# Kernel tuning notes

Hardware: AMD Instinct MI355X
Metric: run time of the kernel (lower is better)

The kernel has to match this reference:

```python
import jax, jax.numpy as jnp
import numpy as np

N = 10000        # nodes
E = 160000       # edges (before self loops)
F_IN = 4         # n_features
D = 128          # d_model (per-head out channels for GAT, GCN width)
H = 8            # n_heads
NEG_SLOPE = 0.2  # PyG GATConv default leaky relu slope


def setup_inputs() -> dict:
    key = jax.random.key(0)
    ks = jax.random.split(key, 10)
    x = jax.random.normal(ks[0], (N, F_IN), dtype=jnp.float32)
    edge_index = jax.random.randint(ks[1], (2, E), 0, N, dtype=jnp.int64)
    s = 0.05
    gat_w = jax.random.normal(ks[2], (F_IN, H * D), dtype=jnp.float32) * s
    att_src = jax.random.normal(ks[3], (H, D), dtype=jnp.float32) * s
    att_dst = jax.random.normal(ks[4], (H, D), dtype=jnp.float32) * s
    gat_b = jnp.zeros((H * D,), dtype=jnp.float32)
    gcn1_w = jax.random.normal(ks[5], (H * D, D), dtype=jnp.float32) * s
    gcn1_b = jnp.zeros((D,), dtype=jnp.float32)
    gcn2_w = jax.random.normal(ks[6], (D, D), dtype=jnp.float32) * s
    gcn2_b = jnp.zeros((D,), dtype=jnp.float32)
    return {"x": x, "edge_index": edge_index, "gat_w": gat_w,
            "att_src": att_src, "att_dst": att_dst, "gat_b": gat_b,
            "gcn1_w": gcn1_w, "gcn1_b": gcn1_b,
            "gcn2_w": gcn2_w, "gcn2_b": gcn2_b}


def _add_self_loops(edge_index, n):
    loops = jnp.arange(n, dtype=edge_index.dtype)
    src = jnp.concatenate([edge_index[0], loops])
    dst = jnp.concatenate([edge_index[1], loops])
    return src, dst


def _gat_conv(x, src, dst, w, att_src, att_dst, b):
    # PyG GATConv, concat=True: h [N,H,D]
    h = (x @ w).reshape(-1, H, D)
    a_s = jnp.einsum('nhd,hd->nh', h, att_src)   # per-node src score
    a_d = jnp.einsum('nhd,hd->nh', h, att_dst)   # per-node dst score
    e = jax.nn.leaky_relu(a_s[src] + a_d[dst], NEG_SLOPE)  # [Etot,H]
    # segment softmax over destination node, per head
    m = jax.ops.segment_max(e, dst, num_segments=N)
    ex = jnp.exp(e - m[dst])
    denom = jax.ops.segment_sum(ex, dst, num_segments=N)
    alpha = ex / denom[dst]                       # [Etot,H]
    msg = h[src] * alpha[:, :, None]              # [Etot,H,D]
    out = jax.ops.segment_sum(msg, dst, num_segments=N)  # [N,H,D]
    return out.reshape(-1, H * D) + b


def _gcn_conv(x, src, dst, w, b):
    # PyG GCNConv with symmetric normalization (self loops already added)
    h = x @ w
    deg = jax.ops.segment_sum(jnp.ones_like(dst, dtype=h.dtype), dst,
                              num_segments=N)
    dinv = jnp.where(deg > 0, jax.lax.rsqrt(deg), 0.0)
    norm = dinv[src] * dinv[dst]                  # [Etot]
    out = jax.ops.segment_sum(h[src] * norm[:, None], dst, num_segments=N)
    return out + b


def reference(x, edge_index, gat_w, att_src, att_dst, gat_b,
              gcn1_w, gcn1_b, gcn2_w, gcn2_b):
    src, dst = _add_self_loops(edge_index, N)
    h = _gat_conv(x, src, dst, gat_w, att_src, att_dst, gat_b)
    h = jax.nn.gelu(h, approximate=False)         # torch F.gelu is exact erf
    h = _gcn_conv(h, src, dst, gcn1_w, gcn1_b)
    h = jax.nn.gelu(h, approximate=False)
    h = _gcn_conv(h, src, dst, gcn2_w, gcn2_b)
    return h                                      # [N, D]
```

## Files before the change

### kernel.cpp

```cpp
#include <hip/hip_runtime.h>
#include <math.h>

#define HEADS 8
#define DHEAD 128
#define CMODEL 1024
#define BCAP 64

typedef __attribute__((ext_vector_type(8))) short bf16x8;
typedef __attribute__((ext_vector_type(4))) float f32x4;

__device__ __forceinline__ float gelu_exact(float x) {
    return 0.5f * x * (1.0f + erff(x * 0.70710678118654752440f));
}

__device__ __forceinline__ unsigned short f2bf(float f) {
    unsigned u = __float_as_uint(f);
    return (unsigned short)((u + 0x7FFFu + ((u >> 16) & 1u)) >> 16);
}
__device__ __forceinline__ float bf2f(unsigned short h) {
    return __uint_as_float((unsigned)h << 16);
}

__global__ void __launch_bounds__(256) k_scores(const float* __restrict__ x,
                                                const float* __restrict__ gat_w,
                                                const float* __restrict__ att_src,
                                                const float* __restrict__ att_dst,
                                                const float* __restrict__ W1,
                                                const float* __restrict__ W2,
                                                float* __restrict__ xpack,
                                                float* __restrict__ a_d,
                                                int* __restrict__ cursor,
                                                unsigned short* __restrict__ W1hi,
                                                unsigned short* __restrict__ W1lo,
                                                unsigned short* __restrict__ W2hi,
                                                unsigned short* __restrict__ W2lo,
                                                int n_nodes, int nb_scores) {
    if ((int)blockIdx.x >= nb_scores) {
        int t = (blockIdx.x - nb_scores) * 256 + threadIdx.x;
        const int total1 = (1024 >> 5) * 8 * 64;
        const int total2 = (128 >> 5) * 8 * 64;
        const float* W; unsigned short *Whi, *Wlo;
        if (t < total1) { W = W1; Whi = W1hi; Wlo = W1lo; }
        else if (t < total1 + total2) { t -= total1; W = W2; Whi = W2hi; Wlo = W2lo; }
        else return;
        int lane = t & 63;
        int ct = (t >> 6) & 7;
        int kc = t >> 9;
        int quad = lane >> 4;
        int col = ct * 16 + (lane & 15);
        size_t o = (size_t)t * 8;
        #pragma unroll
        for (int j = 0; j < 8; j++) {
            float w = W[(size_t)(kc * 32 + quad * 8 + j) * 128 + col];
            unsigned short h = f2bf(w);
            Whi[o + j] = h;
            Wlo[o + j] = f2bf(w - bf2f(h));
        }
        return;
    }
    __shared__ float ws_s[32], ws_d[32];
    int t = threadIdx.x;
    if (t < 64) {
        int e = t >> 1;
        int which = t & 1;
        int hh = e >> 2, k = e & 3;
        const float* wrow = gat_w + k * CMODEL + hh * DHEAD;
        const float* av = which ? (att_dst + hh * DHEAD) : (att_src + hh * DHEAD);
        float s = 0.0f;
        for (int c = 0; c < DHEAD; c++) s += wrow[c] * av[c];
        if (which) ws_d[e] = s; else ws_s[e] = s;
    }
    int gid = blockIdx.x * 256 + t;
    if (gid < n_nodes) cursor[gid] = 0;
    __syncthreads();
    int p = gid;
    if (p >= n_nodes * HEADS) return;
    int n = p >> 3, hh = p & 7;
    float4 xv = *(const float4*)(x + (size_t)n * 4);
    float4 ws = *(const float4*)&ws_s[hh * 4];
    float4 wd = *(const float4*)&ws_d[hh * 4];
    a_d[p] = xv.x * wd.x + xv.y * wd.y + xv.z * wd.z + xv.w * wd.w;
    xpack[(size_t)n * 16 + 4 + hh] =
        xv.x * ws.x + xv.y * ws.y + xv.z * ws.z + xv.w * ws.w;
    if (hh == 0) *(float4*)(xpack + (size_t)n * 16) = xv;
}

__global__ void __launch_bounds__(256) k_scatter(const int* __restrict__ ei,
                                                 int* __restrict__ cursor,
                                                 int* __restrict__ bucket,
                                                 int n_nodes, int n_edges) {
    int e = blockIdx.x * 256 + threadIdx.x;
    int etot = n_edges + n_nodes;
    if (e >= etot) return;
    int s, d;
    if (e < n_edges) { s = ei[e]; d = ei[n_edges + e]; }
    else             { s = d = e - n_edges; }
    int pos = atomicAdd(&cursor[d], 1);
    if (pos < BCAP) bucket[(d << 6) + pos] = s;
}

__global__ void __launch_bounds__(256) k_smax_out1(const float* __restrict__ xpack,
                                                   const float* __restrict__ a_d,
                                                   const int* __restrict__ deg,
                                                   const int* __restrict__ bucket,
                                                   const float* __restrict__ gat_w,
                                                   const float* __restrict__ bias,
                                                   unsigned short* __restrict__ o_hi,
                                                   unsigned short* __restrict__ o_lo,
                                                   int n_nodes) {
    __shared__ float xs[16 * 32];
    int mb = blockIdx.x;
    int t = threadIdx.x;
    int q = t >> 1;
    int half = t & 1;
    int ln = q >> 3, hh = q & 7;
    int n = mb * 16 + ln;
    float sum = 0.0f;
    float4 acc = make_float4(0, 0, 0, 0);
    if (n < n_nodes) {
        int dg = deg[n]; if (dg > BCAP) dg = BCAP;
        int base = n << 6;
        float ad = a_d[n * 8 + hh];
        int r = half;
        for (; r + 6 < dg; r += 8) {
            int s0 = bucket[base + r + 0], s1 = bucket[base + r + 2];
            int s2 = bucket[base + r + 4], s3 = bucket[base + r + 6];
            const float* p0 = xpack + (size_t)s0 * 16;
            const float* p1 = xpack + (size_t)s1 * 16;
            const float* p2 = xpack + (size_t)s2 * 16;
            const float* p3 = xpack + (size_t)s3 * 16;
            float e0 = p0[4 + hh] + ad, e1 = p1[4 + hh] + ad;
            float e2 = p2[4 + hh] + ad, e3 = p3[4 + hh] + ad;
            float4 x0 = *(const float4*)p0;
            float4 x1 = *(const float4*)p1;
            float4 x2 = *(const float4*)p2;
            float4 x3 = *(const float4*)p3;
            e0 = (e0 > 0.0f) ? e0 : 0.2f * e0;  float w0 = __expf(e0);
            e1 = (e1 > 0.0f) ? e1 : 0.2f * e1;  float w1 = __expf(e1);
            e2 = (e2 > 0.0f) ? e2 : 0.2f * e2;  float w2 = __expf(e2);
            e3 = (e3 > 0.0f) ? e3 : 0.2f * e3;  float w3 = __expf(e3);
            sum += w0 + w1 + w2 + w3;
            acc.x += w0 * x0.x + w1 * x1.x + w2 * x2.x + w3 * x3.x;
            acc.y += w0 * x0.y + w1 * x1.y + w2 * x2.y + w3 * x3.y;
            acc.z += w0 * x0.z + w1 * x1.z + w2 * x2.z + w3 * x3.z;
            acc.w += w0 * x0.w + w1 * x1.w + w2 * x2.w + w3 * x3.w;
        }
        for (; r < dg; r += 2) {
            int s = bucket[base + r];
            const float* ps = xpack + (size_t)s * 16;
            float e = ps[4 + hh] + ad;
            e = (e > 0.0f) ? e : 0.2f * e;
            float ex = __expf(e);
            float4 xv = *(const float4*)ps;
            sum += ex;
            acc.x += ex * xv.x; acc.y += ex * xv.y;
            acc.z += ex * xv.z; acc.w += ex * xv.w;
        }
    }
    sum   += __shfl_down(sum, 1);
    acc.x += __shfl_down(acc.x, 1);
    acc.y += __shfl_down(acc.y, 1);
    acc.z += __shfl_down(acc.z, 1);
    acc.w += __shfl_down(acc.w, 1);
    if (half == 0) {
        float inv = (sum > 0.0f) ? (1.0f / sum) : 0.0f;
        *(float4*)&xs[q * 4] = make_float4(acc.x * inv, acc.y * inv,
                                           acc.z * inv, acc.w * inv);
    }
    __syncthreads();
    int lm = t & 15;
    int cb = t >> 4;
    bool valid = (mb * 16 + lm) < n_nodes;
    const float4* w4 = (const float4*)gat_w;
    const float4* b4 = (const float4*)bias;
    #pragma unroll 4
    for (int i = 0; i < 16; i++) {
        int c4 = cb + 16 * i;
        int hh2 = c4 >> 5;
        float4 xa = make_float4(0, 0, 0, 0);
        if (valid) xa = *(const float4*)&xs[(lm * 8 + hh2) * 4];
        float4 w0 = w4[0 * 256 + c4], w1 = w4[1 * 256 + c4],
               w2 = w4[2 * 256 + c4], w3 = w4[3 * 256 + c4];
        float4 bb = b4[c4];
        float v0 = 0, v1 = 0, v2 = 0, v3 = 0;
        if (valid) {
            v0 = gelu_exact(xa.x * w0.x + xa.y * w1.x + xa.z * w2.x + xa.w * w3.x + bb.x);
            v1 = gelu_exact(xa.x * w0.y + xa.y * w1.y + xa.z * w2.y + xa.w * w3.y + bb.y);
            v2 = gelu_exact(xa.x * w0.z + xa.y * w1.z + xa.z * w2.z + xa.w * w3.z + bb.z);
            v3 = gelu_exact(xa.x * w0.w + xa.y * w1.w + xa.z * w2.w + xa.w * w3.w + bb.w);
        }
        int kc = c4 >> 3;
        int quad = (c4 >> 1) & 3;
        int j0 = (c4 & 1) * 4;
        size_t o = (((size_t)mb * 32 + kc) * 64 + quad * 16 + lm) * 8 + j0;
        ushort4 hv, lv;
        unsigned short h;
        h = f2bf(v0); hv.x = h; lv.x = f2bf(v0 - bf2f(h));
        h = f2bf(v1); hv.y = h; lv.y = f2bf(v1 - bf2f(h));
        h = f2bf(v2); hv.z = h; lv.z = f2bf(v2 - bf2f(h));
        h = f2bf(v3); hv.w = h; lv.w = f2bf(v3 - bf2f(h));
        *(ushort4*)(o_hi + o) = hv;
        *(ushort4*)(o_lo + o) = lv;
    }
}

__global__ void __launch_bounds__(256) k_mm_mfma(const unsigned short* __restrict__ Afrag_hi,
                                                 const unsigned short* __restrict__ Afrag_lo,
                                                 const unsigned short* __restrict__ Bhi,
                                                 const unsigned short* __restrict__ Blo,
                                                 const int* __restrict__ deg_scale,
                                                 float* __restrict__ outp,
                                                 int n_nodes, int n_mtiles,
                                                 int kcn, int kc_count) {
    int lane = threadIdx.x & 63;
    int w = threadIdx.x >> 6;
    int colhalf = w >> 1;
    int mtile = blockIdx.x * 2 + (w & 1);
    if (mtile >= n_mtiles) return;
    int kc_begin = blockIdx.y * kc_count;
    outp += (size_t)blockIdx.y * n_nodes * 128;

    int lm = lane & 15, quad = lane >> 4;
    f32x4 acc[4];
    #pragma unroll
    for (int ct = 0; ct < 4; ct++) acc[ct] = (f32x4){0.0f, 0.0f, 0.0f, 0.0f};

    const unsigned short* ah_p = Afrag_hi + (((size_t)mtile * kcn + kc_begin) * 64 + lane) * 8;
    const unsigned short* al_p = Afrag_lo + (((size_t)mtile * kcn + kc_begin) * 64 + lane) * 8;
    const unsigned short* bh_p = Bhi + (((size_t)kc_begin * 8 + colhalf * 4) * 64 + lane) * 8;
    const unsigned short* bl_p = Blo + (((size_t)kc_begin * 8 + colhalf * 4) * 64 + lane) * 8;

    #pragma unroll 4
    for (int kci = 0; kci < kc_count; kci++) {
        bf16x8 ah = *(const bf16x8*)(ah_p + (size_t)kci * 512);
        bf16x8 al = *(const bf16x8*)(al_p + (size_t)kci * 512);
        #pragma unroll
        for (int ct = 0; ct < 4; ct++) {
            bf16x8 bh = *(const bf16x8*)(bh_p + (size_t)kci * 4096 + ct * 512);
            bf16x8 bl = *(const bf16x8*)(bl_p + (size_t)kci * 4096 + ct * 512);
            acc[ct] = __builtin_amdgcn_mfma_f32_16x16x32_bf16(ah, bh, acc[ct], 0, 0, 0);
            acc[ct] = __builtin_amdgcn_mfma_f32_16x16x32_bf16(al, bh, acc[ct], 0, 0, 0);
            acc[ct] = __builtin_amdgcn_mfma_f32_16x16x32_bf16(ah, bl, acc[ct], 0, 0, 0);
        }
    }
    #pragma unroll
    for (int ct = 0; ct < 4; ct++) {
        int col = (colhalf * 4 + ct) * 16 + lm;
        #pragma unroll
        for (int reg = 0; reg < 4; reg++) {
            int row = mtile * 16 + quad * 4 + reg;
            if (row < n_nodes) {
                float v = acc[ct][reg];
                if (deg_scale) v *= 1.0f / sqrtf((float)deg_scale[row]);
                outp[(size_t)row * 128 + col] = v;
            }
        }
    }
}

__global__ void __launch_bounds__(256) k_mm_reduce(const float* __restrict__ part,
                                                   const int* __restrict__ deg,
                                                   float* __restrict__ out,
                                                   int n4, int nsplit) {
    int i = blockIdx.x * 256 + threadIdx.x;
    if (i >= n4) return;
    const float4* p4 = (const float4*)part;
    float4 a = p4[i];
    for (int s = 1; s < nsplit; s++) {
        float4 b = p4[(size_t)s * n4 + i];
        a.x += b.x; a.y += b.y; a.z += b.z; a.w += b.w;
    }
    float dv = 1.0f / sqrtf((float)deg[i >> 5]);
    a.x *= dv; a.y *= dv; a.z *= dv; a.w *= dv;
    ((float4*)out)[i] = a;
}

__global__ void __launch_bounds__(256) k_gcn_agg(const float* __restrict__ t,
                                                 const int* __restrict__ deg,
                                                 const int* __restrict__ bucket,
                                                 const float* __restrict__ bias,
                                                 float* __restrict__ outF,
                                                 unsigned short* __restrict__ outHi,
                                                 unsigned short* __restrict__ outLo,
                                                 int n_nodes, int mode) {
    int c = threadIdx.x & 31;
    int ln = threadIdx.x >> 5;
    int n = blockIdx.x * 8 + ln;
    int col0 = blockIdx.y * 64;
    if (n >= n_nodes) return;
    float2 acc = make_float2(0.0f, 0.0f);
    int dgt = deg[n];
    int dg = dgt > BCAP ? BCAP : dgt;
    int base = n << 6;
    const float* tp = t + col0 + c * 2;
    int r = 0;
    for (; r + 4 <= dg; r += 4) {
        int s0 = bucket[base + r + 0], s1 = bucket[base + r + 1];
        int s2 = bucket[base + r + 2], s3 = bucket[base + r + 3];
        float2 v0 = *(const float2*)(tp + (size_t)s0 * 128);
        float2 v1 = *(const float2*)(tp + (size_t)s1 * 128);
        float2 v2 = *(const float2*)(tp + (size_t)s2 * 128);
        float2 v3 = *(const float2*)(tp + (size_t)s3 * 128);
        acc.x += v0.x + v1.x + v2.x + v3.x;
        acc.y += v0.y + v1.y + v2.y + v3.y;
    }
    for (; r < dg; r++) {
        int s = bucket[base + r];
        float2 v = *(const float2*)(tp + (size_t)s * 128);
        acc.x += v.x; acc.y += v.y;
    }
    float dn = 1.0f / sqrtf((float)dgt);
    int k = col0 + c * 2;
    float2 bb = *(const float2*)(bias + k);
    float vx = acc.x * dn + bb.x;
    float vy = acc.y * dn + bb.y;
    if (mode) {
        vx = gelu_exact(vx); vy = gelu_exact(vy);
        size_t o = (((size_t)(n >> 4) * 4 + (k >> 5)) * 64
                    + ((k >> 3) & 3) * 16 + (n & 15)) * 8 + (k & 7);
        unsigned short hx = f2bf(vx), hy = f2bf(vy);
        outHi[o] = hx; outHi[o + 1] = hy;
        outLo[o] = f2bf(vx - bf2f(hx));
        outLo[o + 1] = f2bf(vy - bf2f(hy));
    } else {
        *(float2*)(outF + (size_t)n * 128 + k) = make_float2(vx, vy);
    }
}

extern "C" void kernel_launch(void* const* d_in, const int* in_sizes, int n_in,
                              void* d_out, int out_size, void* d_ws, size_t ws_size,
                              hipStream_t stream) {
    const float* x        = (const float*)d_in[0];
    const int*   ei       = (const int*)d_in[1];
    const float* gat_w    = (const float*)d_in[2];
    const float* att_src  = (const float*)d_in[3];
    const float* att_dst  = (const float*)d_in[4];
    const float* gat_b    = (const float*)d_in[5];
    const float* gcn1_w   = (const float*)d_in[6];
    const float* gcn1_b   = (const float*)d_in[7];
    const float* gcn2_w   = (const float*)d_in[8];
    const float* gcn2_b   = (const float*)d_in[9];
    float* out = (float*)d_out;

    int N = in_sizes[0] / 4;
    int E = in_sizes[1] / 2;
    int Etot = E + N;
    int n_mtiles = (N + 15) / 16;

    char* base = (char*)d_ws;
    float*          t      = (float*)(base);
    float*          t2     = (float*)(base + 5120000);
    unsigned short* out2hi = (unsigned short*)(base + 10240000);
    unsigned short* out2lo = (unsigned short*)(base + 12800000);
    float*          part   = (float*)(base + 15360000);
    unsigned short* w1hi   = (unsigned short*)(base + 26000000);
    unsigned short* w1lo   = (unsigned short*)(base + 26262144);
    unsigned short* w2hi   = (unsigned short*)(base + 26524288);
    unsigned short* w2lo   = (unsigned short*)(base + 26557056);
    unsigned short* out1hi = (unsigned short*)(base + 40960000);
    unsigned short* out1lo = (unsigned short*)(base + 61440000);
    size_t off = 81920000;
    float* xpack  = (float*)(base + off); off += (size_t)N * 16 * 4;
    float* a_d    = (float*)(base + off); off += (size_t)N * 8 * 4;
    int*   cursor = (int*)(base + off);   off += (size_t)N * 4;
    int*   bucket = (int*)(base + off);   off += (size_t)N * BCAP * 4;

    int nb_scores = (N * HEADS + 255) / 256;
    int nb_wswz   = (16384 + 2048 + 255) / 256;

    k_scores<<<nb_scores + nb_wswz, 256, 0, stream>>>(x, gat_w, att_src, att_dst,
                                                      gcn1_w, gcn2_w, xpack, a_d, cursor,
                                                      w1hi, w1lo, w2hi, w2lo, N, nb_scores);

    k_scatter<<<(Etot + 255) / 256, 256, 0, stream>>>(ei, cursor, bucket, N, E);

    k_smax_out1<<<n_mtiles, 256, 0, stream>>>(xpack, a_d, cursor, bucket,
                                              gat_w, gat_b, out1hi, out1lo, N);

    int nmb2 = (n_mtiles + 1) / 2;
    int n4 = N * 32;
    int nagg = (N + 7) / 8;

    k_mm_mfma<<<dim3(nmb2, 2), 256, 0, stream>>>(out1hi, out1lo, w1hi, w1lo,
                                                 nullptr, part, N, n_mtiles, 32, 16);
    k_mm_reduce<<<(n4 + 255) / 256, 256, 0, stream>>>(part, cursor, t, n4, 2);

    k_gcn_agg<<<dim3(nagg, 2), 256, 0, stream>>>(t, cursor, bucket, gcn1_b,
                                                 nullptr, out2hi, out2lo, N, 1);

    k_mm_mfma<<<dim3(nmb2, 1), 256, 0, stream>>>(out2hi, out2lo, w2hi, w2lo,
                                                 (const int*)cursor, t2, N, n_mtiles, 4, 4);

    k_gcn_agg<<<dim3(nagg, 2), 256, 0, stream>>>(t2, cursor, bucket, gcn2_b,
                                                 out, nullptr, nullptr, N, 0);
}
```

Measured before the change: 173.4 us.

## Fuse all stages into one cooperative persistent kernel with grid syncs

```diff
diff --git a/kernel.cpp b/kernel.cpp
--- a/kernel.cpp
+++ b/kernel.cpp
@@ -1,5 +1,8 @@
 #include <hip/hip_runtime.h>
+#include <hip/hip_cooperative_groups.h>
 #include <math.h>
+
+namespace cg = cooperative_groups;
 
 #define HEADS 8
 #define DHEAD 128
@@ -12,7 +15,6 @@
 __device__ __forceinline__ float gelu_exact(float x) {
     return 0.5f * x * (1.0f + erff(x * 0.70710678118654752440f));
 }
-
 __device__ __forceinline__ unsigned short f2bf(float f) {
     unsigned u = __float_as_uint(f);
     return (unsigned short)((u + 0x7FFFu + ((u >> 16) & 1u)) >> 16);
@@ -21,114 +23,101 @@
     return __uint_as_float((unsigned)h << 16);
 }
 
-__global__ void __launch_bounds__(256) k_scores(const float* __restrict__ x,
-                                                const float* __restrict__ gat_w,
-                                                const float* __restrict__ att_src,
-                                                const float* __restrict__ att_dst,
-                                                const float* __restrict__ W1,
-                                                const float* __restrict__ W2,
-                                                float* __restrict__ xpack,
-                                                float* __restrict__ a_d,
-                                                int* __restrict__ cursor,
-                                                unsigned short* __restrict__ W1hi,
-                                                unsigned short* __restrict__ W1lo,
-                                                unsigned short* __restrict__ W2hi,
-                                                unsigned short* __restrict__ W2lo,
-                                                int n_nodes, int nb_scores) {
-    if ((int)blockIdx.x >= nb_scores) {
-        int t = (blockIdx.x - nb_scores) * 256 + threadIdx.x;
-        const int total1 = (1024 >> 5) * 8 * 64;
-        const int total2 = (128 >> 5) * 8 * 64;
-        const float* W; unsigned short *Whi, *Wlo;
-        if (t < total1) { W = W1; Whi = W1hi; Wlo = W1lo; }
-        else if (t < total1 + total2) { t -= total1; W = W2; Whi = W2hi; Wlo = W2lo; }
-        else return;
-        int lane = t & 63;
-        int ct = (t >> 6) & 7;
-        int kc = t >> 9;
-        int quad = lane >> 4;
-        int col = ct * 16 + (lane & 15);
-        size_t o = (size_t)t * 8;
-        #pragma unroll
-        for (int j = 0; j < 8; j++) {
-            float w = W[(size_t)(kc * 32 + quad * 8 + j) * 128 + col];
-            unsigned short h = f2bf(w);
-            Whi[o + j] = h;
-            Wlo[o + j] = f2bf(w - bf2f(h));
-        }
-        return;
-    }
-    __shared__ float ws_s[32], ws_d[32];
-    int t = threadIdx.x;
-    if (t < 64) {
-        int e = t >> 1;
-        int which = t & 1;
+struct MegaArgs {
+    const float* x; const int* ei;
+    const float* gat_w; const float* att_src; const float* att_dst; const float* gat_b;
+    const float* gcn1_w; const float* gcn1_b; const float* gcn2_w; const float* gcn2_b;
+    float* out;
+    float* t; float* t2;
+    unsigned short* out2hi; unsigned short* out2lo;
+    float* part;
+    unsigned short* w1hi; unsigned short* w1lo;
+    unsigned short* w2hi; unsigned short* w2lo;
+    unsigned short* out1hi; unsigned short* out1lo;
+    float* xpack; float* a_d; int* cursor; int* bucket;
+    int N, E;
+};
+
+
+__device__ void ph_scores(const MegaArgs& a, int job, int tid, float* sh) {
+    float* ws_s = sh; float* ws_d = sh + 32;
+    if (tid < 64) {
+        int e = tid >> 1, which = tid & 1;
         int hh = e >> 2, k = e & 3;
-        const float* wrow = gat_w + k * CMODEL + hh * DHEAD;
-        const float* av = which ? (att_dst + hh * DHEAD) : (att_src + hh * DHEAD);
+        const float* wrow = a.gat_w + k * CMODEL + hh * DHEAD;
+        const float* av = which ? (a.att_dst + hh * DHEAD) : (a.att_src + hh * DHEAD);
         float s = 0.0f;
         for (int c = 0; c < DHEAD; c++) s += wrow[c] * av[c];
         if (which) ws_d[e] = s; else ws_s[e] = s;
     }
-    int gid = blockIdx.x * 256 + t;
-    if (gid < n_nodes) cursor[gid] = 0;
+    int gid = job * 256 + tid;
+    if (gid < a.N) a.cursor[gid] = 0;
     __syncthreads();
     int p = gid;
-    if (p >= n_nodes * HEADS) return;
-    int n = p >> 3, hh = p & 7;
-    float4 xv = *(const float4*)(x + (size_t)n * 4);
-    float4 ws = *(const float4*)&ws_s[hh * 4];
-    float4 wd = *(const float4*)&ws_d[hh * 4];
-    a_d[p] = xv.x * wd.x + xv.y * wd.y + xv.z * wd.z + xv.w * wd.w;
-    xpack[(size_t)n * 16 + 4 + hh] =
-        xv.x * ws.x + xv.y * ws.y + xv.z * ws.z + xv.w * ws.w;
-    if (hh == 0) *(float4*)(xpack + (size_t)n * 16) = xv;
-}
-
-__global__ void __launch_bounds__(256) k_scatter(const int* __restrict__ ei,
-                                                 int* __restrict__ cursor,
-                                                 int* __restrict__ bucket,
-                                                 int n_nodes, int n_edges) {
-    int e = blockIdx.x * 256 + threadIdx.x;
-    int etot = n_edges + n_nodes;
+    if (p < a.N * HEADS) {
+        int n = p >> 3, hh = p & 7;
+        float4 xv = *(const float4*)(a.x + (size_t)n * 4);
+        float4 ws = *(const float4*)&ws_s[hh * 4];
+        float4 wd = *(const float4*)&ws_d[hh * 4];
+        a.a_d[p] = xv.x * wd.x + xv.y * wd.y + xv.z * wd.z + xv.w * wd.w;
+        a.xpack[(size_t)n * 16 + 4 + hh] =
+            xv.x * ws.x + xv.y * ws.y + xv.z * ws.z + xv.w * ws.w;
+        if (hh == 0) *(float4*)(a.xpack + (size_t)n * 16) = xv;
+    }
+    __syncthreads();
+}
+
+__device__ void ph_wswz(const MegaArgs& a, int t) {
+    const int total1 = (1024 >> 5) * 8 * 64;
+    const int total2 = (128 >> 5) * 8 * 64;
+    const float* W; unsigned short *Whi, *Wlo;
+    if (t < total1) { W = a.gcn1_w; Whi = a.w1hi; Wlo = a.w1lo; }
+    else if (t < total1 + total2) { t -= total1; W = a.gcn2_w; Whi = a.w2hi; Wlo = a.w2lo; }
+    else return;
+    int lane = t & 63;
+    int ct = (t >> 6) & 7;
+    int kc = t >> 9;
+    int quad = lane >> 4;
+    int col = ct * 16 + (lane & 15);
+    size_t o = (size_t)t * 8;
+    #pragma unroll
+    for (int j = 0; j < 8; j++) {
+        float w = W[(size_t)(kc * 32 + quad * 8 + j) * 128 + col];
+        unsigned short h = f2bf(w);
+        Whi[o + j] = h;
+        Wlo[o + j] = f2bf(w - bf2f(h));
+    }
+}
+
+__device__ void ph_scatter(const MegaArgs& a, int job, int tid) {
+    int e = job * 256 + tid;
+    int etot = a.E + a.N;
     if (e >= etot) return;
     int s, d;
-    if (e < n_edges) { s = ei[e]; d = ei[n_edges + e]; }
-    else             { s = d = e - n_edges; }
-    int pos = atomicAdd(&cursor[d], 1);
-    if (pos < BCAP) bucket[(d << 6) + pos] = s;
-}
-
-__global__ void __launch_bounds__(256) k_smax_out1(const float* __restrict__ xpack,
-                                                   const float* __restrict__ a_d,
-                                                   const int* __restrict__ deg,
-                                                   const int* __restrict__ bucket,
-                                                   const float* __restrict__ gat_w,
-                                                   const float* __restrict__ bias,
-                                                   unsigned short* __restrict__ o_hi,
-                                                   unsigned short* __restrict__ o_lo,
-                                                   int n_nodes) {
-    __shared__ float xs[16 * 32];
-    int mb = blockIdx.x;
-    int t = threadIdx.x;
-    int q = t >> 1;
-    int half = t & 1;
+    if (e < a.E) { s = a.ei[e]; d = a.ei[a.E + e]; }
+    else         { s = d = e - a.E; }
+    int pos = atomicAdd(&a.cursor[d], 1);
+    if (pos < BCAP) a.bucket[(d << 6) + pos] = s;
+}
+
+__device__ void ph_smax_out1(const MegaArgs& a, int mb, int t, float* xs) {
+    int q = t >> 1, half = t & 1;
     int ln = q >> 3, hh = q & 7;
     int n = mb * 16 + ln;
     float sum = 0.0f;
     float4 acc = make_float4(0, 0, 0, 0);
-    if (n < n_nodes) {
-        int dg = deg[n]; if (dg > BCAP) dg = BCAP;
+    if (n < a.N) {
+        int dg = a.cursor[n]; if (dg > BCAP) dg = BCAP;
         int base = n << 6;
-        float ad = a_d[n * 8 + hh];
+        float ad = a.a_d[n * 8 + hh];
         int r = half;
         for (; r + 6 < dg; r += 8) {
-            int s0 = bucket[base + r + 0], s1 = bucket[base + r + 2];
-            int s2 = bucket[base + r + 4], s3 = bucket[base + r + 6];
-            const float* p0 = xpack + (size_t)s0 * 16;
-            const float* p1 = xpack + (size_t)s1 * 16;
-            const float* p2 = xpack + (size_t)s2 * 16;
-            const float* p3 = xpack + (size_t)s3 * 16;
+            int s0 = a.bucket[base + r + 0], s1 = a.bucket[base + r + 2];
+            int s2 = a.bucket[base + r + 4], s3 = a.bucket[base + r + 6];
+            const float* p0 = a.xpack + (size_t)s0 * 16;
+            const float* p1 = a.xpack + (size_t)s1 * 16;
+            const float* p2 = a.xpack + (size_t)s2 * 16;
+            const float* p3 = a.xpack + (size_t)s3 * 16;
             float e0 = p0[4 + hh] + ad, e1 = p1[4 + hh] + ad;
             float e2 = p2[4 + hh] + ad, e3 = p3[4 + hh] + ad;
             float4 x0 = *(const float4*)p0;
@@ -146,8 +135,8 @@
             acc.w += w0 * x0.w + w1 * x1.w + w2 * x2.w + w3 * x3.w;
         }
         for (; r < dg; r += 2) {
-            int s = bucket[base + r];
-            const float* ps = xpack + (size_t)s * 16;
+            int s = a.bucket[base + r];
+            const float* ps = a.xpack + (size_t)s * 16;
             float e = ps[4 + hh] + ad;
             e = (e > 0.0f) ? e : 0.2f * e;
             float ex = __expf(e);
@@ -170,9 +159,9 @@
     __syncthreads();
     int lm = t & 15;
     int cb = t >> 4;
-    bool valid = (mb * 16 + lm) < n_nodes;
-    const float4* w4 = (const float4*)gat_w;
-    const float4* b4 = (const float4*)bias;
+    bool valid = (mb * 16 + lm) < a.N;
+    const float4* w4 = (const float4*)a.gat_w;
+    const float4* b4 = (const float4*)a.gat_b;
     #pragma unroll 4
     for (int i = 0; i < 16; i++) {
         int c4 = cb + 16 * i;
@@ -199,34 +188,32 @@
         h = f2bf(v1); hv.y = h; lv.y = f2bf(v1 - bf2f(h));
         h = f2bf(v2); hv.z = h; lv.z = f2bf(v2 - bf2f(h));
         h = f2bf(v3); hv.w = h; lv.w = f2bf(v3 - bf2f(h));
-        *(ushort4*)(o_hi + o) = hv;
-        *(ushort4*)(o_lo + o) = lv;
-    }
-}
-
-__global__ void __launch_bounds__(256) k_mm_mfma(const unsigned short* __restrict__ Afrag_hi,
-                                                 const unsigned short* __restrict__ Afrag_lo,
-                                                 const unsigned short* __restrict__ Bhi,
-                                                 const unsigned short* __restrict__ Blo,
-                                                 const int* __restrict__ deg_scale,
-                                                 float* __restrict__ outp,
-                                                 int n_nodes, int n_mtiles,
-                                                 int kcn, int kc_count) {
-    int lane = threadIdx.x & 63;
-    int w = threadIdx.x >> 6;
+        *(ushort4*)(a.out1hi + o) = hv;
+        *(ushort4*)(a.out1lo + o) = lv;
+    }
+    __syncthreads();
+}
+
+__device__ void ph_mm(const unsigned short* Ahi, const unsigned short* Alo,
+                      const unsigned short* Bhi, const unsigned short* Blo,
+                      const int* deg_scale, float* outp,
+                      int n_nodes, int n_mtiles, int kcn, int kc_count,
+                      int bx, int ksplit, int tid) {
+    int lane = tid & 63;
+    int w = tid >> 6;
     int colhalf = w >> 1;
-    int mtile = blockIdx.x * 2 + (w & 1);
+    int mtile = bx * 2 + (w & 1);
     if (mtile >= n_mtiles) return;
-    int kc_begin = blockIdx.y * kc_count;
-    outp += (size_t)blockIdx.y * n_nodes * 128;
+    int kc_begin = ksplit * kc_count;
+    outp += (size_t)ksplit * n_nodes * 128;
 
     int lm = lane & 15, quad = lane >> 4;
     f32x4 acc[4];
     #pragma unroll
     for (int ct = 0; ct < 4; ct++) acc[ct] = (f32x4){0.0f, 0.0f, 0.0f, 0.0f};
 
-    const unsigned short* ah_p = Afrag_hi + (((size_t)mtile * kcn + kc_begin) * 64 + lane) * 8;
-    const unsigned short* al_p = Afrag_lo + (((size_t)mtile * kcn + kc_begin) * 64 + lane) * 8;
+    const unsigned short* ah_p = Ahi + (((size_t)mtile * kcn + kc_begin) * 64 + lane) * 8;
+    const unsigned short* al_p = Alo + (((size_t)mtile * kcn + kc_begin) * 64 + lane) * 8;
     const unsigned short* bh_p = Bhi + (((size_t)kc_begin * 8 + colhalf * 4) * 64 + lane) * 8;
     const unsigned short* bl_p = Blo + (((size_t)kc_begin * 8 + colhalf * 4) * 64 + lane) * 8;
 
@@ -258,45 +245,35 @@
     }
 }
 
-__global__ void __launch_bounds__(256) k_mm_reduce(const float* __restrict__ part,
-                                                   const int* __restrict__ deg,
-                                                   float* __restrict__ out,
-                                                   int n4, int nsplit) {
-    int i = blockIdx.x * 256 + threadIdx.x;
+__device__ void ph_reduce(const MegaArgs& a, int job, int tid, int n4) {
+    int i = job * 256 + tid;
     if (i >= n4) return;
-    const float4* p4 = (const float4*)part;
-    float4 a = p4[i];
-    for (int s = 1; s < nsplit; s++) {
-        float4 b = p4[(size_t)s * n4 + i];
-        a.x += b.x; a.y += b.y; a.z += b.z; a.w += b.w;
-    }
-    float dv = 1.0f / sqrtf((float)deg[i >> 5]);
-    a.x *= dv; a.y *= dv; a.z *= dv; a.w *= dv;
-    ((float4*)out)[i] = a;
-}
-
-__global__ void __launch_bounds__(256) k_gcn_agg(const float* __restrict__ t,
-                                                 const int* __restrict__ deg,
-                                                 const int* __restrict__ bucket,
-                                                 const float* __restrict__ bias,
-                                                 float* __restrict__ outF,
-                                                 unsigned short* __restrict__ outHi,
-                                                 unsigned short* __restrict__ outLo,
-                                                 int n_nodes, int mode) {
-    int c = threadIdx.x & 31;
-    int ln = threadIdx.x >> 5;
-    int n = blockIdx.x * 8 + ln;
-    int col0 = blockIdx.y * 64;
-    if (n >= n_nodes) return;
+    const float4* p4 = (const float4*)a.part;
+    float4 v = p4[i];
+    float4 b = p4[(size_t)n4 + i];
+    v.x += b.x; v.y += b.y; v.z += b.z; v.w += b.w;
+    float dv = 1.0f / sqrtf((float)a.cursor[i >> 5]);
+    v.x *= dv; v.y *= dv; v.z *= dv; v.w *= dv;
+    ((float4*)a.t)[i] = v;
+}
+
+__device__ void ph_gcn_agg(const MegaArgs& a, const float* t, const float* bias,
+                           float* outF, unsigned short* outHi, unsigned short* outLo,
+                           int mode, int bx, int colh, int tid) {
+    int c = tid & 31;
+    int ln = tid >> 5;
+    int n = bx * 8 + ln;
+    int col0 = colh * 64;
+    if (n >= a.N) return;
     float2 acc = make_float2(0.0f, 0.0f);
-    int dgt = deg[n];
+    int dgt = a.cursor[n];
     int dg = dgt > BCAP ? BCAP : dgt;
     int base = n << 6;
     const float* tp = t + col0 + c * 2;
     int r = 0;
     for (; r + 4 <= dg; r += 4) {
-        int s0 = bucket[base + r + 0], s1 = bucket[base + r + 1];
-        int s2 = bucket[base + r + 2], s3 = bucket[base + r + 3];
+        int s0 = a.bucket[base + r + 0], s1 = a.bucket[base + r + 1];
+        int s2 = a.bucket[base + r + 2], s3 = a.bucket[base + r + 3];
         float2 v0 = *(const float2*)(tp + (size_t)s0 * 128);
         float2 v1 = *(const float2*)(tp + (size_t)s1 * 128);
         float2 v2 = *(const float2*)(tp + (size_t)s2 * 128);
@@ -305,7 +282,7 @@
         acc.y += v0.y + v1.y + v2.y + v3.y;
     }
     for (; r < dg; r++) {
-        int s = bucket[base + r];
+        int s = a.bucket[base + r];
         float2 v = *(const float2*)(tp + (size_t)s * 128);
         acc.x += v.x; acc.y += v.y;
     }
@@ -327,70 +304,91 @@
     }
 }
 
+__global__ void __launch_bounds__(256, 2) k_mega(MegaArgs a) {
+    cg::grid_group grid = cg::this_grid();
+    __shared__ float sh[16 * 32];
+    const int nb = gridDim.x;
+    const int tid = threadIdx.x;
+    const int N = a.N;
+    const int Etot = a.E + N;
+    const int n_mtiles = (N + 15) / 16;
+    const int nb_scores = (N * HEADS + 255) / 256;
+    const int nb_wswz = (16384 + 2048 + 255) / 256;
+    const int nb_scatter = (Etot + 255) / 256;
+    const int nmb2 = (n_mtiles + 1) / 2;
+    const int n4 = N * 32;
+    const int nb_red = (n4 + 255) / 256;
+    const int nagg = (N + 7) / 8;
+
+    for (int job = blockIdx.x; job < nb_scores + nb_wswz; job += nb) {
+        if (job < nb_scores) ph_scores(a, job, tid, sh);
+        else                 ph_wswz(a, (job - nb_scores) * 256 + tid);
+    }
+    grid.sync();
+    for (int job = blockIdx.x; job < nb_scatter; job += nb)
+        ph_scatter(a, job, tid);
+    grid.sync();
+    for (int job = blockIdx.x; job < n_mtiles; job += nb)
+        ph_smax_out1(a, job, tid, sh);
+    grid.sync();
+    for (int job = blockIdx.x; job < nmb2 * 2; job += nb)
+        ph_mm(a.out1hi, a.out1lo, a.w1hi, a.w1lo, nullptr, a.part,
+              N, n_mtiles, 32, 16, job % nmb2, job / nmb2, tid);
+    grid.sync();
+    for (int job = blockIdx.x; job < nb_red; job += nb)
+        ph_reduce(a, job, tid, n4);
+    grid.sync();
+    for (int job = blockIdx.x; job < nagg * 2; job += nb)
+        ph_gcn_agg(a, a.t, a.gcn1_b, nullptr, a.out2hi, a.out2lo, 1,
+                   job % nagg, job / nagg, tid);
+    grid.sync();
+    for (int job = blockIdx.x; job < nmb2; job += nb)
+        ph_mm(a.out2hi, a.out2lo, a.w2hi, a.w2lo, a.cursor, a.t2,
+              N, n_mtiles, 4, 4, job, 0, tid);
+    grid.sync();
+    for (int job = blockIdx.x; job < nagg * 2; job += nb)
+        ph_gcn_agg(a, a.t2, a.gcn2_b, a.out, nullptr, nullptr, 0,
+                   job % nagg, job / nagg, tid);
+}
+
 extern "C" void kernel_launch(void* const* d_in, const int* in_sizes, int n_in,
                               void* d_out, int out_size, void* d_ws, size_t ws_size,
                               hipStream_t stream) {
-    const float* x        = (const float*)d_in[0];
-    const int*   ei       = (const int*)d_in[1];
-    const float* gat_w    = (const float*)d_in[2];
-    const float* att_src  = (const float*)d_in[3];
-    const float* att_dst  = (const float*)d_in[4];
-    const float* gat_b    = (const float*)d_in[5];
-    const float* gcn1_w   = (const float*)d_in[6];
-    const float* gcn1_b   = (const float*)d_in[7];
-    const float* gcn2_w   = (const float*)d_in[8];
-    const float* gcn2_b   = (const float*)d_in[9];
-    float* out = (float*)d_out;
-
     int N = in_sizes[0] / 4;
     int E = in_sizes[1] / 2;
-    int Etot = E + N;
-    int n_mtiles = (N + 15) / 16;
 
     char* base = (char*)d_ws;
-    float*          t      = (float*)(base);
-    float*          t2     = (float*)(base + 5120000);
-    unsigned short* out2hi = (unsigned short*)(base + 10240000);
-    unsigned short* out2lo = (unsigned short*)(base + 12800000);
-    float*          part   = (float*)(base + 15360000);
-    unsigned short* w1hi   = (unsigned short*)(base + 26000000);
-    unsigned short* w1lo   = (unsigned short*)(base + 26262144);
-    unsigned short* w2hi   = (unsigned short*)(base + 26524288);
-    unsigned short* w2lo   = (unsigned short*)(base + 26557056);
-    unsigned short* out1hi = (unsigned short*)(base + 40960000);
-    unsigned short* out1lo = (unsigned short*)(base + 61440000);
+    MegaArgs a;
+    a.x       = (const float*)d_in[0];
+    a.ei      = (const int*)d_in[1];
+    a.gat_w   = (const float*)d_in[2];
+    a.att_src = (const float*)d_in[3];
+    a.att_dst = (const float*)d_in[4];
+    a.gat_b   = (const float*)d_in[5];
+    a.gcn1_w  = (const float*)d_in[6];
+    a.gcn1_b  = (const float*)d_in[7];
+    a.gcn2_w  = (const float*)d_in[8];
+    a.gcn2_b  = (const float*)d_in[9];
+    a.out     = (float*)d_out;
+    a.t       = (float*)(base);
+    a.t2      = (float*)(base + 5120000);
+    a.out2hi  = (unsigned short*)(base + 10240000);
+    a.out2lo  = (unsigned short*)(base + 12800000);
+    a.part    = (float*)(base + 15360000);
+    a.w1hi    = (unsigned short*)(base + 26000000);
+    a.w1lo    = (unsigned short*)(base + 26262144);
+    a.w2hi    = (unsigned short*)(base + 26524288);
+    a.w2lo    = (unsigned short*)(base + 26557056);
+    a.out1hi  = (unsigned short*)(base + 40960000);
+    a.out1lo  = (unsigned short*)(base + 61440000);
     size_t off = 81920000;
-    float* xpack  = (float*)(base + off); off += (size_t)N * 16 * 4;
-    float* a_d    = (float*)(base + off); off += (size_t)N * 8 * 4;
-    int*   cursor = (int*)(base + off);   off += (size_t)N * 4;
-    int*   bucket = (int*)(base + off);   off += (size_t)N * BCAP * 4;
-
-    int nb_scores = (N * HEADS + 255) / 256;
-    int nb_wswz   = (16384 + 2048 + 255) / 256;
-
-    k_scores<<<nb_scores + nb_wswz, 256, 0, stream>>>(x, gat_w, att_src, att_dst,
-                                                      gcn1_w, gcn2_w, xpack, a_d, cursor,
-                                                      w1hi, w1lo, w2hi, w2lo, N, nb_scores);
-
-    k_scatter<<<(Etot + 255) / 256, 256, 0, stream>>>(ei, cursor, bucket, N, E);
-
-    k_smax_out1<<<n_mtiles, 256, 0, stream>>>(xpack, a_d, cursor, bucket,
-                                              gat_w, gat_b, out1hi, out1lo, N);
-
-    int nmb2 = (n_mtiles + 1) / 2;
-    int n4 = N * 32;
-    int nagg = (N + 7) / 8;
-
-    k_mm_mfma<<<dim3(nmb2, 2), 256, 0, stream>>>(out1hi, out1lo, w1hi, w1lo,
-                                                 nullptr, part, N, n_mtiles, 32, 16);
-    k_mm_reduce<<<(n4 + 255) / 256, 256, 0, stream>>>(part, cursor, t, n4, 2);
-
-    k_gcn_agg<<<dim3(nagg, 2), 256, 0, stream>>>(t, cursor, bucket, gcn1_b,
-                                                 nullptr, out2hi, out2lo, N, 1);
-
-    k_mm_mfma<<<dim3(nmb2, 1), 256, 0, stream>>>(out2hi, out2lo, w2hi, w2lo,
-                                                 (const int*)cursor, t2, N, n_mtiles, 4, 4);
-
-    k_gcn_agg<<<dim3(nagg, 2), 256, 0, stream>>>(t2, cursor, bucket, gcn2_b,
-                                                 out, nullptr, nullptr, N, 0);
-}
+    a.xpack   = (float*)(base + off); off += (size_t)N * 16 * 4;
+    a.a_d     = (float*)(base + off); off += (size_t)N * 8 * 4;
+    a.cursor  = (int*)(base + off);   off += (size_t)N * 4;
+    a.bucket  = (int*)(base + off);   off += (size_t)N * BCAP * 4;
+    a.N = N; a.E = E;
+
+    void* kargs[] = { &a };
+    hipLaunchCooperativeKernel((void*)k_mega, dim3(512), dim3(256),
+                               kargs, 0, stream);
+}
```

New measurement: 631.1 us. 264% more time.

## Fuse first GCN aggregation with second GCN matmul in one kernel

Applied to the files above, without the earlier changes.

```diff
diff --git a/kernel.cpp b/kernel.cpp
--- a/kernel.cpp
+++ b/kernel.cpp
@@ -26,23 +26,16 @@
                                                 const float* __restrict__ att_src,
                                                 const float* __restrict__ att_dst,
                                                 const float* __restrict__ W1,
-                                                const float* __restrict__ W2,
                                                 float* __restrict__ xpack,
                                                 float* __restrict__ a_d,
                                                 int* __restrict__ cursor,
                                                 unsigned short* __restrict__ W1hi,
                                                 unsigned short* __restrict__ W1lo,
-                                                unsigned short* __restrict__ W2hi,
-                                                unsigned short* __restrict__ W2lo,
                                                 int n_nodes, int nb_scores) {
     if ((int)blockIdx.x >= nb_scores) {
         int t = (blockIdx.x - nb_scores) * 256 + threadIdx.x;
         const int total1 = (1024 >> 5) * 8 * 64;
-        const int total2 = (128 >> 5) * 8 * 64;
-        const float* W; unsigned short *Whi, *Wlo;
-        if (t < total1) { W = W1; Whi = W1hi; Wlo = W1lo; }
-        else if (t < total1 + total2) { t -= total1; W = W2; Whi = W2hi; Wlo = W2lo; }
-        else return;
+        if (t >= total1) return;
         int lane = t & 63;
         int ct = (t >> 6) & 7;
         int kc = t >> 9;
@@ -51,10 +44,10 @@
         size_t o = (size_t)t * 8;
         #pragma unroll
         for (int j = 0; j < 8; j++) {
-            float w = W[(size_t)(kc * 32 + quad * 8 + j) * 128 + col];
+            float w = W1[(size_t)(kc * 32 + quad * 8 + j) * 128 + col];
             unsigned short h = f2bf(w);
-            Whi[o + j] = h;
-            Wlo[o + j] = f2bf(w - bf2f(h));
+            W1hi[o + j] = h;
+            W1lo[o + j] = f2bf(w - bf2f(h));
         }
         return;
     }
@@ -208,7 +201,6 @@
                                                  const unsigned short* __restrict__ Afrag_lo,
                                                  const unsigned short* __restrict__ Bhi,
                                                  const unsigned short* __restrict__ Blo,
-                                                 const int* __restrict__ deg_scale,
                                                  float* __restrict__ outp,
                                                  int n_nodes, int n_mtiles,
                                                  int kcn, int kc_count) {
@@ -249,11 +241,8 @@
         #pragma unroll
         for (int reg = 0; reg < 4; reg++) {
             int row = mtile * 16 + quad * 4 + reg;
-            if (row < n_nodes) {
-                float v = acc[ct][reg];
-                if (deg_scale) v *= 1.0f / sqrtf((float)deg_scale[row]);
-                outp[(size_t)row * 128 + col] = v;
-            }
+            if (row < n_nodes)
+                outp[(size_t)row * 128 + col] = acc[ct][reg];
         }
     }
 }
@@ -275,14 +264,76 @@
     ((float4*)out)[i] = a;
 }
 
+__global__ void __launch_bounds__(256) k_agg1_mm2(const float* __restrict__ t,
+                                                  const int* __restrict__ deg,
+                                                  const int* __restrict__ bucket,
+                                                  const float* __restrict__ b1,
+                                                  const float* __restrict__ W2,
+                                                  float* __restrict__ t2,
+                                                  int n_nodes) {
+    __shared__ float o2[8 * 128];
+    int c = threadIdx.x & 31;
+    int ln = threadIdx.x >> 5;
+    int n = blockIdx.x * 8 + ln;
+    bool valid = (n < n_nodes);
+    float4 acc = make_float4(0, 0, 0, 0);
+    float dn = 0.0f;
+    if (valid) {
+        int dgt = deg[n];
+        int dg = dgt > BCAP ? BCAP : dgt;
+        int base = n << 6;
+        const float* tp = t + c * 4;
+        int r = 0;
+        for (; r + 4 <= dg; r += 4) {
+            int s0 = bucket[base + r + 0], s1 = bucket[base + r + 1];
+            int s2 = bucket[base + r + 2], s3 = bucket[base + r + 3];
+            float4 v0 = *(const float4*)(tp + (size_t)s0 * 128);
+            float4 v1 = *(const float4*)(tp + (size_t)s1 * 128);
+            float4 v2 = *(const float4*)(tp + (size_t)s2 * 128);
+            float4 v3 = *(const float4*)(tp + (size_t)s3 * 128);
+            acc.x += v0.x + v1.x + v2.x + v3.x;
+            acc.y += v0.y + v1.y + v2.y + v3.y;
+            acc.z += v0.z + v1.z + v2.z + v3.z;
+            acc.w += v0.w + v1.w + v2.w + v3.w;
+        }
+        for (; r < dg; r++) {
+            int s = bucket[base + r];
+            float4 v = *(const float4*)(tp + (size_t)s * 128);
+            acc.x += v.x; acc.y += v.y; acc.z += v.z; acc.w += v.w;
+        }
+        dn = 1.0f / sqrtf((float)dgt);
+        float4 bb = *(const float4*)(b1 + c * 4);
+        acc.x = gelu_exact(acc.x * dn + bb.x);
+        acc.y = gelu_exact(acc.y * dn + bb.y);
+        acc.z = gelu_exact(acc.z * dn + bb.z);
+        acc.w = gelu_exact(acc.w * dn + bb.w);
+    }
+    *(float4*)&o2[ln * 128 + c * 4] = acc;
+    __syncthreads();
+    if (!valid) return;
+    float4 r0 = make_float4(0, 0, 0, 0), r1 = make_float4(0, 0, 0, 0);
+    const float* wp = W2 + c * 4;
+    #pragma unroll 4
+    for (int k = 0; k < 128; k += 2) {
+        float a0 = o2[ln * 128 + k];
+        float a1 = o2[ln * 128 + k + 1];
+        float4 w0 = *(const float4*)(wp + (size_t)k * 128);
+        float4 w1 = *(const float4*)(wp + (size_t)(k + 1) * 128);
+        r0.x += a0 * w0.x; r0.y += a0 * w0.y; r0.z += a0 * w0.z; r0.w += a0 * w0.w;
+        r1.x += a1 * w1.x; r1.y += a1 * w1.y; r1.z += a1 * w1.z; r1.w += a1 * w1.w;
+    }
+    float4 rr;
+    rr.x = (r0.x + r1.x) * dn; rr.y = (r0.y + r1.y) * dn;
+    rr.z = (r0.z + r1.z) * dn; rr.w = (r0.w + r1.w) * dn;
+    *(float4*)(t2 + (size_t)n * 128 + c * 4) = rr;
+}
+
 __global__ void __launch_bounds__(256) k_gcn_agg(const float* __restrict__ t,
                                                  const int* __restrict__ deg,
                                                  const int* __restrict__ bucket,
                                                  const float* __restrict__ bias,
                                                  float* __restrict__ outF,
-                                                 unsigned short* __restrict__ outHi,
-                                                 unsigned short* __restrict__ outLo,
-                                                 int n_nodes, int mode) {
+                                                 int n_nodes) {
     int c = threadIdx.x & 31;
     int ln = threadIdx.x >> 5;
     int n = blockIdx.x * 8 + ln;
@@ -312,19 +363,8 @@
     float dn = 1.0f / sqrtf((float)dgt);
     int k = col0 + c * 2;
     float2 bb = *(const float2*)(bias + k);
-    float vx = acc.x * dn + bb.x;
-    float vy = acc.y * dn + bb.y;
-    if (mode) {
-        vx = gelu_exact(vx); vy = gelu_exact(vy);
-        size_t o = (((size_t)(n >> 4) * 4 + (k >> 5)) * 64
-                    + ((k >> 3) & 3) * 16 + (n & 15)) * 8 + (k & 7);
-        unsigned short hx = f2bf(vx), hy = f2bf(vy);
-        outHi[o] = hx; outHi[o + 1] = hy;
-        outLo[o] = f2bf(vx - bf2f(hx));
-        outLo[o + 1] = f2bf(vy - bf2f(hy));
-    } else {
-        *(float2*)(outF + (size_t)n * 128 + k) = make_float2(vx, vy);
-    }
+    *(float2*)(outF + (size_t)n * 128 + k) =
+        make_float2(acc.x * dn + bb.x, acc.y * dn + bb.y);
 }
 
 extern "C" void kernel_launch(void* const* d_in, const int* in_sizes, int n_in,
@@ -350,13 +390,9 @@
     char* base = (char*)d_ws;
     float*          t      = (float*)(base);
     float*          t2     = (float*)(base + 5120000);
-    unsigned short* out2hi = (unsigned short*)(base + 10240000);
-    unsigned short* out2lo = (unsigned short*)(base + 12800000);
     float*          part   = (float*)(base + 15360000);
     unsigned short* w1hi   = (unsigned short*)(base + 26000000);
     unsigned short* w1lo   = (unsigned short*)(base + 26262144);
-    unsigned short* w2hi   = (unsigned short*)(base + 26524288);
-    unsigned short* w2lo   = (unsigned short*)(base + 26557056);
     unsigned short* out1hi = (unsigned short*)(base + 40960000);
     unsigned short* out1lo = (unsigned short*)(base + 61440000);
     size_t off = 81920000;
@@ -366,11 +402,11 @@
     int*   bucket = (int*)(base + off);   off += (size_t)N * BCAP * 4;
 
     int nb_scores = (N * HEADS + 255) / 256;
-    int nb_wswz   = (16384 + 2048 + 255) / 256;
+    int nb_wswz   = (16384 + 255) / 256;
 
     k_scores<<<nb_scores + nb_wswz, 256, 0, stream>>>(x, gat_w, att_src, att_dst,
-                                                      gcn1_w, gcn2_w, xpack, a_d, cursor,
-                                                      w1hi, w1lo, w2hi, w2lo, N, nb_scores);
+                                                      gcn1_w, xpack, a_d, cursor,
+                                                      w1hi, w1lo, N, nb_scores);
 
     k_scatter<<<(Etot + 255) / 256, 256, 0, stream>>>(ei, cursor, bucket, N, E);
 
@@ -382,15 +418,11 @@
     int nagg = (N + 7) / 8;
 
     k_mm_mfma<<<dim3(nmb2, 2), 256, 0, stream>>>(out1hi, out1lo, w1hi, w1lo,
-                                                 nullptr, part, N, n_mtiles, 32, 16);
+                                                 part, N, n_mtiles, 32, 16);
+
     k_mm_reduce<<<(n4 + 255) / 256, 256, 0, stream>>>(part, cursor, t, n4, 2);
 
-    k_gcn_agg<<<dim3(nagg, 2), 256, 0, stream>>>(t, cursor, bucket, gcn1_b,
-                                                 nullptr, out2hi, out2lo, N, 1);
-
-    k_mm_mfma<<<dim3(nmb2, 1), 256, 0, stream>>>(out2hi, out2lo, w2hi, w2lo,
-                                                 (const int*)cursor, t2, N, n_mtiles, 4, 4);
-
-    k_gcn_agg<<<dim3(nagg, 2), 256, 0, stream>>>(t2, cursor, bucket, gcn2_b,
-                                                 out, nullptr, nullptr, N, 0);
-}
+    k_agg1_mm2<<<nagg, 256, 0, stream>>>(t, cursor, bucket, gcn1_b, gcn2_w, t2, N);
+
+    k_gcn_agg<<<dim3(nagg, 2), 256, 0, stream>>>(t2, cursor, bucket, gcn2_b, out, N);
+}
```

After: 176.9 us. 2.0% more time.
